# Kernel optimization log

Hardware: AMD Instinct MI355X
Metric: run time of the kernel (lower is better)

The kernel has to match this reference:

```python
import jax, jax.numpy as jnp
import numpy as np

DIM, H, DH, MLP, ADIM = 512, 8, 64, 2048, 256
B, T = 4, 2048
EPS = 1e-5


def setup_inputs() -> dict:
    key = jax.random.key(0)
    ks = jax.random.split(key, 10)
    s = 0.02
    inner = H * DH
    return {
        "x": jax.random.normal(ks[0], (B, T, DIM), jnp.float32),
        "action_emb": jax.random.normal(ks[1], (B, T, ADIM), jnp.float32),
        "causal_mask": jnp.tril(jnp.ones((T, T), dtype=bool)),
        "Wqkv": jax.random.normal(ks[2], (3 * inner, DIM), jnp.float32) * s,
        "Wout": jax.random.normal(ks[3], (DIM, inner), jnp.float32) * s,
        "bout": jnp.zeros((DIM,), jnp.float32),
        "W1": jax.random.normal(ks[4], (MLP, DIM), jnp.float32) * s,
        "b1": jnp.zeros((MLP,), jnp.float32),
        "W2": jax.random.normal(ks[5], (DIM, MLP), jnp.float32) * s,
        "b2": jnp.zeros((DIM,), jnp.float32),
        # adaLN is zero-init in the module; use small random so modulation is exercised
        "Wmod": jax.random.normal(ks[6], (6 * DIM, ADIM), jnp.float32) * s,
        "bmod": jnp.zeros((6 * DIM,), jnp.float32),
    }


def _layernorm(z):
    mu = jnp.mean(z, axis=-1, keepdims=True)
    var = jnp.var(z, axis=-1, keepdims=True)
    return (z - mu) * jax.lax.rsqrt(var + EPS)


def reference(x, action_emb, causal_mask, Wqkv, Wout, bout, W1, b1, W2, b2, Wmod, bmod):
    b, t, d = x.shape
    mod = jax.nn.silu(action_emb) @ Wmod.T + bmod            # (B,T,6*dim)
    shift1, scale1, gate1, shift2, scale2, gate2 = jnp.split(mod, 6, axis=-1)

    h = _layernorm(x) * (1.0 + scale1) + shift1
    qkv = (h @ Wqkv.T).reshape(b, t, 3, H, DH)
    q, k, v = qkv[:, :, 0], qkv[:, :, 1], qkv[:, :, 2]        # (B,T,H,DH)
    scores = jnp.einsum("bqhd,bkhd->bhqk", q, k) * (DH ** -0.5)
    scores = jnp.where(causal_mask, scores, -jnp.inf)
    attn = jax.nn.softmax(scores, axis=-1)                   # dropout=eval (identity)
    h = jnp.einsum("bhqk,bkhd->bqhd", attn, v).reshape(b, t, H * DH)
    h = h @ Wout.T + bout
    x = x + gate1 * h

    h = _layernorm(x) * (1.0 + scale2) + shift2
    h = jax.nn.gelu(h @ W1.T + b1, approximate=False) @ W2.T + b2
    return x + gate2 * h
```

## Files before the change

kernel.cpp:

```cpp
#include <hip/hip_runtime.h>
#include <math.h>
#include <stdint.h>

#define BB 4
#define TT 2048
#define NTOK 8192
#define DIMD 512
#define HH 8
#define DHH 64
#define MLPD 2048
#define ADIMD 256
#define MODD 3072
#define LNEPS 1e-5f
#define LOG2E_8 0.18033688011112042f

typedef short short8 __attribute__((ext_vector_type(8)));
typedef unsigned short ushort4v __attribute__((ext_vector_type(4)));
typedef __bf16 bf16x8 __attribute__((ext_vector_type(8)));
typedef float f32x4 __attribute__((ext_vector_type(4)));

static __device__ __forceinline__ unsigned short f2bf(float f) {
    union { float f; unsigned u; } v; v.f = f;
    unsigned r = v.u + 0x7fffu + ((v.u >> 16) & 1u);
    return (unsigned short)(r >> 16);
}
static __device__ __forceinline__ float bf2f(unsigned short u) {
    union { unsigned u; float f; } v; v.u = (unsigned)u << 16; return v.f;
}
static __device__ __forceinline__ unsigned pk2bf(float a, float b) {
    return (unsigned)f2bf(a) | ((unsigned)f2bf(b) << 16);
}

static __device__ __forceinline__ f32x4 mfma_bf16(short8 a, short8 b, f32x4 c) {
    return __builtin_amdgcn_mfma_f32_16x16x32_bf16(
        __builtin_bit_cast(bf16x8, a), __builtin_bit_cast(bf16x8, b), c, 0, 0, 0);
}

struct CvtArgs {
    const float* s[6];
    unsigned short* d[6];
    int cum[7];
};
__global__ __launch_bounds__(256) void cvt_all(CvtArgs a)
{
    const int i = blockIdx.x * 256 + threadIdx.x;
    if (i >= a.cum[6]) return;
    int seg = 0;
    #pragma unroll
    for (int k = 1; k < 6; k++) seg += (i >= a.cum[k]);
    const int off = i - a.cum[seg];
    float4 v = ((const float4*)a.s[seg])[off];
    if (seg == 5) {
        v.x = v.x / (1.f + __expf(-v.x));
        v.y = v.y / (1.f + __expf(-v.y));
        v.z = v.z / (1.f + __expf(-v.z));
        v.w = v.w / (1.f + __expf(-v.w));
    }
    uint2 o;
    o.x = pk2bf(v.x, v.y);
    o.y = pk2bf(v.z, v.w);
    ((uint2*)a.d[seg])[off] = o;
}

template<int EPI, int BN>
__global__ __launch_bounds__(256, (BN == 128 ? 3 : 4)) void gemm_bf16(
    const unsigned short* __restrict__ A, const unsigned short* __restrict__ Bw,
    const float* __restrict__ bias, const float* __restrict__ res,
    const unsigned short* __restrict__ mod,
    int M, int N, int K,
    void* __restrict__ Cv)
{
    constexpr int MT = (BN == 128) ? 4 : 2;
    constexpr int NPB = (BN == 128) ? 4 : 2;
    __shared__ unsigned short As[128 * 72];
    __shared__ unsigned short Bs[BN * 72];

    const int tid = threadIdx.x;
    const int w = tid >> 6, lane = tid & 63;
    const int quad = lane >> 4, l16 = lane & 15;
    const int wrow = (BN == 128) ? (w >> 1) * 64 : w * 32;
    const int wcol = (BN == 128) ? (w & 1) * 64 : 0;
    const int row0 = blockIdx.y * 128, col0 = blockIdx.x * BN;

    const int srow = tid >> 3;
    const int skc  = (tid & 7) * 8;

    f32x4 acc[MT][4];
    #pragma unroll
    for (int i = 0; i < MT; i++)
        #pragma unroll
        for (int j = 0; j < 4; j++) acc[i][j] = (f32x4){0.f, 0.f, 0.f, 0.f};

    short8 pA[4], pB[NPB];
    auto prefetch = [&](int k0) {
        #pragma unroll
        for (int p = 0; p < 4; p++)
            pA[p] = *(const short8*)&A[(size_t)(row0 + srow + p * 32) * K + k0 + skc];
        #pragma unroll
        for (int p = 0; p < NPB; p++)
            pB[p] = *(const short8*)&Bw[(size_t)(col0 + srow + p * 32) * K + k0 + skc];
    };
    auto stage = [&]() {
        #pragma unroll
        for (int p = 0; p < 4; p++)
            *(short8*)&As[(srow + p * 32) * 72 + skc] = pA[p];
        #pragma unroll
        for (int p = 0; p < NPB; p++)
            *(short8*)&Bs[(srow + p * 32) * 72 + skc] = pB[p];
    };

    prefetch(0);
    stage();
    __syncthreads();

    for (int k0 = 0; k0 < K; k0 += 64) {
        const bool more = (k0 + 64 < K);
        if (more) prefetch(k0 + 64);

        #pragma unroll
        for (int ks = 0; ks < 2; ks++) {
            short8 af[MT], bf[4];
            #pragma unroll
            for (int mt = 0; mt < MT; mt++)
                af[mt] = *(const short8*)&As[(wrow + mt * 16 + l16) * 72 + ks * 32 + quad * 8];
            #pragma unroll
            for (int nt = 0; nt < 4; nt++)
                bf[nt] = *(const short8*)&Bs[(wcol + nt * 16 + l16) * 72 + ks * 32 + quad * 8];
            #pragma unroll
            for (int nt = 0; nt < 4; nt++)
                #pragma unroll
                for (int mt = 0; mt < MT; mt++)
                    acc[mt][nt] = mfma_bf16(af[mt], bf[nt], acc[mt][nt]);
        }
        __syncthreads();
        if (more) stage();
        __syncthreads();
    }

    float* Cf = (float*)Cv;
    unsigned short* Cb = (unsigned short*)Cv;
    #pragma unroll
    for (int mt = 0; mt < MT; mt++) {
        #pragma unroll
        for (int r = 0; r < 4; r++) {
            const int row = row0 + wrow + mt * 16 + quad * 4 + r;
            #pragma unroll
            for (int nt = 0; nt < 4; nt++) {
                const int col = col0 + wcol + nt * 16 + l16;
                const size_t idx = (size_t)row * N + col;
                const float v = acc[mt][nt][r];
                if (EPI == 0) {
                    Cb[idx] = f2bf(v);
                } else if (EPI == 2) {
                    float t = v + bias[col];
                    Cb[idx] = f2bf(0.5f * t * (1.f + erff(t * 0.70710678118654752f)));
                } else if (EPI == 3) {
                    float t = v + bias[col];
                    Cf[idx] = res[idx] + bf2f(mod[(size_t)row * MODD + 1024 + col]) * t;
                } else if (EPI == 4) {
                    float t = v + bias[col];
                    Cf[idx] = Cf[idx] + bf2f(mod[(size_t)row * MODD + 2560 + col]) * t;
                } else if (EPI == 5) {
                    Cb[idx] = f2bf(v + bias[col]);
                }
            }
        }
    }
}

__global__ __launch_bounds__(256) void adaln_ln(
    const float* __restrict__ src, const unsigned short* __restrict__ mod,
    unsigned short* __restrict__ dst, int shift_off, int scale_off)
{
    const int n = blockIdx.x;
    const int tid = threadIdx.x;
    const float* xr = src + (size_t)n * DIMD;
    float v0 = xr[tid], v1 = xr[tid + 256];
    float s = v0 + v1;
    float q = v0 * v0 + v1 * v1;
    #pragma unroll
    for (int o = 32; o > 0; o >>= 1) {
        s += __shfl_down(s, o);
        q += __shfl_down(q, o);
    }
    __shared__ float sh[8];
    __shared__ float mu_sh, rs_sh;
    const int wid = tid >> 6, lane = tid & 63;
    if (lane == 0) { sh[wid] = s; sh[wid + 4] = q; }
    __syncthreads();
    if (tid == 0) {
        float S = sh[0] + sh[1] + sh[2] + sh[3];
        float Q = sh[4] + sh[5] + sh[6] + sh[7];
        float mu = S * (1.f / DIMD);
        float var = Q * (1.f / DIMD) - mu * mu;
        mu_sh = mu;
        rs_sh = rsqrtf(var + LNEPS);
    }
    __syncthreads();
    const float mu = mu_sh, rs = rs_sh;
    const unsigned short* mrow = mod + (size_t)n * MODD;
    const size_t o0 = (size_t)n * DIMD + tid;
    dst[o0]       = f2bf((v0 - mu) * rs * (1.f + bf2f(mrow[scale_off + tid]))       + bf2f(mrow[shift_off + tid]));
    dst[o0 + 256] = f2bf((v1 - mu) * rs * (1.f + bf2f(mrow[scale_off + tid + 256])) + bf2f(mrow[shift_off + tid + 256]));
}

__global__ __launch_bounds__(256, 4) void attn_mfma(
    const unsigned short* __restrict__ qkv, unsigned short* __restrict__ outb)
{
    __shared__ unsigned short Kt[64][72];
    __shared__ unsigned short Vt[64][72];
    __shared__ unsigned short Ps[4][16][72];

    const int qi = (TT / 64 - 1) - blockIdx.x;
    const int h = blockIdx.y, b = blockIdx.z;
    const int tid = threadIdx.x;
    const int w = tid >> 6;
    const int lane = tid & 63;
    const int quad = lane >> 4;
    const int l16 = lane & 15;

    const int qw = qi * 64 + w * 16;
    const size_t tokbase = (size_t)b * TT;

    short8 qf[2];
    {
        const unsigned short* qp = qkv + (tokbase + qw + l16) * 1536 + h * 64 + quad * 8;
        #pragma unroll
        for (int hd = 0; hd < 2; hd++) {
            short8 raw = *(const short8*)(qp + hd * 32);
            short8 f;
            #pragma unroll
            for (int j = 0; j < 8; j++)
                f[j] = (short)f2bf(bf2f((unsigned short)raw[j]) * LOG2E_8);
            qf[hd] = f;
        }
    }

    f32x4 Oa[4];
    float mrun = -INFINITY, lrun = 0.f;
    #pragma unroll
    for (int mt = 0; mt < 4; mt++) Oa[mt] = (f32x4){0.f, 0.f, 0.f, 0.f};

    const int nkt = qi + 1;
    const int vk0 = (tid & 31) * 2;
    const int vdb = (tid >> 5) * 8;

    short8 kpre[2], vpre[2];
    auto prefetchKV = [&](int kt) {
        const unsigned short* kb = qkv + (tokbase + (size_t)kt * 64) * 1536 + 512 + h * 64;
        #pragma unroll
        for (int it = 0; it < 2; it++) {
            const int i = tid + it * 256;
            kpre[it] = *(const short8*)(kb + (size_t)(i >> 3) * 1536 + (i & 7) * 8);
        }
        const unsigned short* vb = qkv + (tokbase + (size_t)kt * 64 + vk0) * 1536 + 1024 + h * 64 + vdb;
        vpre[0] = *(const short8*)vb;
        vpre[1] = *(const short8*)(vb + 1536);
    };
    auto storeKV = [&]() {
        #pragma unroll
        for (int it = 0; it < 2; it++) {
            const int i = tid + it * 256;
            *(short8*)&Kt[i >> 3][(i & 7) * 8] = kpre[it];
        }
        #pragma unroll
        for (int j = 0; j < 8; j++) {
            *(unsigned*)&Vt[vdb + j][vk0] =
                (unsigned)(unsigned short)vpre[0][j]
                | ((unsigned)(unsigned short)vpre[1][j] << 16);
        }
    };

    prefetchKV(0);
    storeKV();
    __syncthreads();

    for (int kt = 0; kt < nkt; kt++) {
        const bool haveNext = (kt + 1 < nkt);
        if (haveNext) prefetchKV(kt + 1);

        f32x4 st[4];
        #pragma unroll
        for (int mk = 0; mk < 4; mk++) {
            const short8 a0 = *(const short8*)&Kt[mk * 16 + l16][quad * 8];
            const short8 a1 = *(const short8*)&Kt[mk * 16 + l16][32 + quad * 8];
            st[mk] = (f32x4){0.f, 0.f, 0.f, 0.f};
            st[mk] = mfma_bf16(a0, qf[0], st[mk]);
            st[mk] = mfma_bf16(a1, qf[1], st[mk]);
        }
        if (kt == qi) {
            const int qpos = qw + l16;
            #pragma unroll
            for (int mk = 0; mk < 4; mk++)
                #pragma unroll
                for (int r = 0; r < 4; r++)
                    if (kt * 64 + mk * 16 + quad * 4 + r > qpos) st[mk][r] = -INFINITY;
        }
        float tm = -INFINITY;
        #pragma unroll
        for (int mk = 0; mk < 4; mk++)
            #pragma unroll
            for (int r = 0; r < 4; r++) tm = fmaxf(tm, st[mk][r]);
        tm = fmaxf(tm, __shfl_xor(tm, 16));
        tm = fmaxf(tm, __shfl_xor(tm, 32));
        const float mn = fmaxf(mrun, tm);
        const float alpha = __builtin_amdgcn_exp2f(mrun - mn);
        mrun = mn;
        float ts = 0.f;
        #pragma unroll
        for (int mk = 0; mk < 4; mk++) {
            const float p0 = __builtin_amdgcn_exp2f(st[mk][0] - mn);
            const float p1 = __builtin_amdgcn_exp2f(st[mk][1] - mn);
            const float p2 = __builtin_amdgcn_exp2f(st[mk][2] - mn);
            const float p3 = __builtin_amdgcn_exp2f(st[mk][3] - mn);
            ts += (p0 + p1) + (p2 + p3);
            const unsigned long long pk =
                (unsigned long long)pk2bf(p0, p1)
                | ((unsigned long long)pk2bf(p2, p3) << 32);
            *(unsigned long long*)&Ps[w][l16][mk * 16 + quad * 4] = pk;
        }
        ts += __shfl_xor(ts, 16);
        ts += __shfl_xor(ts, 32);
        lrun = lrun * alpha + ts;
        #pragma unroll
        for (int mt = 0; mt < 4; mt++) Oa[mt] *= alpha;
        __threadfence_block();

        short8 pf[2];
        #pragma unroll
        for (int kc = 0; kc < 2; kc++)
            pf[kc] = *(const short8*)&Ps[w][l16][kc * 32 + quad * 8];
        #pragma unroll
        for (int mt = 0; mt < 4; mt++)
            #pragma unroll
            for (int kc = 0; kc < 2; kc++) {
                const short8 vf = *(const short8*)&Vt[mt * 16 + l16][kc * 32 + quad * 8];
                Oa[mt] = mfma_bf16(vf, pf[kc], Oa[mt]);
            }

        __syncthreads();
        if (haveNext) storeKV();
        __syncthreads();
    }

    {
        const float inv = 1.f / lrun;
        const size_t tok = tokbase + qw + l16;
        #pragma unroll
        for (int mt = 0; mt < 4; mt++) {
            const unsigned long long pk =
                (unsigned long long)pk2bf(Oa[mt][0] * inv, Oa[mt][1] * inv)
                | ((unsigned long long)pk2bf(Oa[mt][2] * inv, Oa[mt][3] * inv) << 32);
            *(unsigned long long*)&outb[tok * DIMD + h * 64 + mt * 16 + quad * 4] = pk;
        }
    }
}

extern "C" void kernel_launch(void* const* d_in, const int* in_sizes, int n_in,
                              void* d_out, int out_size, void* d_ws, size_t ws_size,
                              hipStream_t stream)
{
    (void)in_sizes; (void)n_in; (void)out_size; (void)ws_size;

    const float* x    = (const float*)d_in[0];
    const float* aemb = (const float*)d_in[1];
    const float* Wqkv = (const float*)d_in[3];
    const float* Wout = (const float*)d_in[4];
    const float* bout = (const float*)d_in[5];
    const float* W1   = (const float*)d_in[6];
    const float* b1   = (const float*)d_in[7];
    const float* W2   = (const float*)d_in[8];
    const float* b2   = (const float*)d_in[9];
    const float* Wmod = (const float*)d_in[10];
    const float* bmod = (const float*)d_in[11];

    float* out = (float*)d_out;

    char* p = (char*)d_ws;
    unsigned short* modw = (unsigned short*)p; p += (size_t)NTOK * MODD * 2;
    unsigned short* h12  = (unsigned short*)p; p += (size_t)NTOK * DIMD * 2;
    unsigned short* qkvb = (unsigned short*)p; p += (size_t)NTOK * 1536 * 2;
    unsigned short* attw = (unsigned short*)p; p += (size_t)NTOK * DIMD * 2;
    unsigned short* hid  = qkvb;
    unsigned short* sact = (unsigned short*)p; p += (size_t)NTOK * ADIMD * 2;
    unsigned short* wq = (unsigned short*)p;   p += (size_t)1536 * 512 * 2;
    unsigned short* wo = (unsigned short*)p;   p += (size_t)512 * 512 * 2;
    unsigned short* w1 = (unsigned short*)p;   p += (size_t)2048 * 512 * 2;
    unsigned short* w2 = (unsigned short*)p;   p += (size_t)512 * 2048 * 2;
    unsigned short* wm = (unsigned short*)p;   p += (size_t)3072 * 256 * 2;

    CvtArgs ca;
    ca.s[0] = Wqkv; ca.d[0] = wq;
    ca.s[1] = Wout; ca.d[1] = wo;
    ca.s[2] = W1;   ca.d[2] = w1;
    ca.s[3] = W2;   ca.d[3] = w2;
    ca.s[4] = Wmod; ca.d[4] = wm;
    ca.s[5] = aemb; ca.d[5] = sact;
    const int n4s[6] = {1536 * 512 / 4, 512 * 512 / 4, 2048 * 512 / 4,
                        512 * 2048 / 4, 3072 * 256 / 4, NTOK * ADIMD / 4};
    ca.cum[0] = 0;
    for (int i = 0; i < 6; i++) ca.cum[i + 1] = ca.cum[i] + n4s[i];
    cvt_all<<<(ca.cum[6] + 255) / 256, 256, 0, stream>>>(ca);

    gemm_bf16<5, 128><<<dim3(MODD / 128, NTOK / 128), 256, 0, stream>>>(
        sact, wm, bmod, nullptr, nullptr, NTOK, MODD, ADIMD, modw);

    adaln_ln<<<NTOK, 256, 0, stream>>>(x, modw, h12, 0, 512);

    gemm_bf16<0, 128><<<dim3(1536 / 128, NTOK / 128), 256, 0, stream>>>(
        h12, wq, nullptr, nullptr, nullptr, NTOK, 1536, DIMD, qkvb);

    attn_mfma<<<dim3(TT / 64, HH, BB), 256, 0, stream>>>(qkvb, attw);

    gemm_bf16<3, 64><<<dim3(DIMD / 64, NTOK / 128), 256, 0, stream>>>(
        attw, wo, bout, x, modw, NTOK, DIMD, DIMD, out);

    adaln_ln<<<NTOK, 256, 0, stream>>>(out, modw, h12, 1536, 2048);

    gemm_bf16<2, 128><<<dim3(MLPD / 128, NTOK / 128), 256, 0, stream>>>(
        h12, w1, b1, nullptr, nullptr, NTOK, MLPD, DIMD, hid);

    gemm_bf16<4, 64><<<dim3(DIMD / 64, NTOK / 128), 256, 0, stream>>>(
        hid, w2, b2, nullptr, modw, NTOK, DIMD, MLPD, out);
}
```

Measured before the change: 330.7 us.

## Split causal attention KV range into chunks with a separate combine kernel

Each query tile's causal key range is split into chunks of up to 8 key tiles, giving 80 work items per (batch, head) instead of 32 tiles of very unequal length. Each chunk writes unnormalized fp32 partial outputs plus running max and sum to workspace, and a new combine kernel merges them with log-sum-exp rescaling into the bf16 attention output. The LDS row padding in the GEMM and attention kernels also changes from 72 to 76 to alter bank mapping. The split aims to cut the long tail from the longest causal rows, at the cost of extra fp32 partial traffic, an additional kernel launch, and possible misaligned 16-byte LDS accesses with the new stride.

```diff
diff --git a/kernel.cpp b/kernel.cpp
--- a/kernel.cpp
+++ b/kernel.cpp
@@ -13,6 +13,7 @@
 #define MODD 3072
 #define LNEPS 1e-5f
 #define LOG2E_8 0.18033688011112042f
+#define PBLK 4224
 
 typedef short short8 __attribute__((ext_vector_type(8)));
 typedef unsigned short ushort4v __attribute__((ext_vector_type(4)));
@@ -72,8 +73,8 @@
 {
     constexpr int MT = (BN == 128) ? 4 : 2;
     constexpr int NPB = (BN == 128) ? 4 : 2;
-    __shared__ unsigned short As[128 * 72];
-    __shared__ unsigned short Bs[BN * 72];
+    __shared__ unsigned short As[128 * 76];
+    __shared__ unsigned short Bs[BN * 76];
 
     const int tid = threadIdx.x;
     const int w = tid >> 6, lane = tid & 63;
@@ -103,10 +104,10 @@
     auto stage = [&]() {
         #pragma unroll
         for (int p = 0; p < 4; p++)
-            *(short8*)&As[(srow + p * 32) * 72 + skc] = pA[p];
+            *(short8*)&As[(srow + p * 32) * 76 + skc] = pA[p];
         #pragma unroll
         for (int p = 0; p < NPB; p++)
-            *(short8*)&Bs[(srow + p * 32) * 72 + skc] = pB[p];
+            *(short8*)&Bs[(srow + p * 32) * 76 + skc] = pB[p];
     };
 
     prefetch(0);
@@ -122,10 +123,10 @@
             short8 af[MT], bf[4];
             #pragma unroll
             for (int mt = 0; mt < MT; mt++)
-                af[mt] = *(const short8*)&As[(wrow + mt * 16 + l16) * 72 + ks * 32 + quad * 8];
+                af[mt] = *(const short8*)&As[(wrow + mt * 16 + l16) * 76 + ks * 32 + quad * 8];
             #pragma unroll
             for (int nt = 0; nt < 4; nt++)
-                bf[nt] = *(const short8*)&Bs[(wcol + nt * 16 + l16) * 72 + ks * 32 + quad * 8];
+                bf[nt] = *(const short8*)&Bs[(wcol + nt * 16 + l16) * 76 + ks * 32 + quad * 8];
             #pragma unroll
             for (int nt = 0; nt < 4; nt++)
                 #pragma unroll
@@ -205,13 +206,19 @@
 }
 
 __global__ __launch_bounds__(256, 4) void attn_mfma(
-    const unsigned short* __restrict__ qkv, unsigned short* __restrict__ outb)
-{
-    __shared__ unsigned short Kt[64][72];
-    __shared__ unsigned short Vt[64][72];
-    __shared__ unsigned short Ps[4][16][72];
-
-    const int qi = (TT / 64 - 1) - blockIdx.x;
+    const unsigned short* __restrict__ qkv, float* __restrict__ part)
+{
+    __shared__ unsigned short Kt[64][76];
+    __shared__ unsigned short Vt[64][76];
+    __shared__ unsigned short Ps[4][16][76];
+
+    const int f = 79 - (int)blockIdx.x;
+    int qi, ch;
+    if (f < 8)       { qi = f;               ch = 0; }
+    else if (f < 24) { const int g = f - 8;  qi = 8 + (g >> 1);  ch = g & 1; }
+    else if (f < 48) { const int g = f - 24; qi = 16 + g / 3;    ch = g % 3; }
+    else             { const int g = f - 48; qi = 24 + (g >> 2); ch = g & 3; }
+
     const int h = blockIdx.y, b = blockIdx.z;
     const int tid = threadIdx.x;
     const int w = tid >> 6;
@@ -228,11 +235,11 @@
         #pragma unroll
         for (int hd = 0; hd < 2; hd++) {
             short8 raw = *(const short8*)(qp + hd * 32);
-            short8 f;
+            short8 fr;
             #pragma unroll
             for (int j = 0; j < 8; j++)
-                f[j] = (short)f2bf(bf2f((unsigned short)raw[j]) * LOG2E_8);
-            qf[hd] = f;
+                fr[j] = (short)f2bf(bf2f((unsigned short)raw[j]) * LOG2E_8);
+            qf[hd] = fr;
         }
     }
 
@@ -241,7 +248,8 @@
     #pragma unroll
     for (int mt = 0; mt < 4; mt++) Oa[mt] = (f32x4){0.f, 0.f, 0.f, 0.f};
 
-    const int nkt = qi + 1;
+    const int k0t = ch * 8;
+    const int k1t = min(k0t + 8, qi + 1);
     const int vk0 = (tid & 31) * 2;
     const int vdb = (tid >> 5) * 8;
 
@@ -271,12 +279,12 @@
         }
     };
 
-    prefetchKV(0);
+    prefetchKV(k0t);
     storeKV();
     __syncthreads();
 
-    for (int kt = 0; kt < nkt; kt++) {
-        const bool haveNext = (kt + 1 < nkt);
+    for (int kt = k0t; kt < k1t; kt++) {
+        const bool haveNext = (kt + 1 < k1t);
         if (haveNext) prefetchKV(kt + 1);
 
         f32x4 st[4];
@@ -289,12 +297,12 @@
             st[mk] = mfma_bf16(a1, qf[1], st[mk]);
         }
         if (kt == qi) {
-            const int qpos = qw + l16;
+            const int qrel = w * 16 + l16;
             #pragma unroll
             for (int mk = 0; mk < 4; mk++)
                 #pragma unroll
                 for (int r = 0; r < 4; r++)
-                    if (kt * 64 + mk * 16 + quad * 4 + r > qpos) st[mk][r] = -INFINITY;
+                    if (mk * 16 + quad * 4 + r > qrel) st[mk][r] = -INFINITY;
         }
         float tm = -INFINITY;
         #pragma unroll
@@ -343,17 +351,52 @@
         __syncthreads();
     }
 
-    {
-        const float inv = 1.f / lrun;
-        const size_t tok = tokbase + qw + l16;
-        #pragma unroll
-        for (int mt = 0; mt < 4; mt++) {
-            const unsigned long long pk =
-                (unsigned long long)pk2bf(Oa[mt][0] * inv, Oa[mt][1] * inv)
-                | ((unsigned long long)pk2bf(Oa[mt][2] * inv, Oa[mt][3] * inv) << 32);
-            *(unsigned long long*)&outb[tok * DIMD + h * 64 + mt * 16 + quad * 4] = pk;
-        }
-    }
+    float* pO = part + ((size_t)((b * HH + h) * 80 + f)) * PBLK;
+    #pragma unroll
+    for (int mt = 0; mt < 4; mt++)
+        *(f32x4*)&pO[(w * 16 + l16) * 64 + mt * 16 + quad * 4] = Oa[mt];
+    if (quad == 0) {
+        pO[4096 + (w * 16 + l16) * 2]     = mrun;
+        pO[4096 + (w * 16 + l16) * 2 + 1] = lrun;
+    }
+}
+
+__global__ __launch_bounds__(256) void attn_combine(
+    const float* __restrict__ part, unsigned short* __restrict__ outb)
+{
+    const int idx = blockIdx.x * 256 + threadIdx.x;
+    const int d4 = idx & 15;
+    const int h = (idx >> 4) & 7;
+    const int tok = idx >> 7;
+    const int t = tok & (TT - 1);
+    const int b = tok >> 11;
+    const int qi = t >> 6;
+    const int nch = (qi >> 3) + 1;
+    int cum;
+    if (qi < 8)       cum = qi;
+    else if (qi < 16) cum = 8 + ((qi - 8) << 1);
+    else if (qi < 24) cum = 24 + (qi - 16) * 3;
+    else              cum = 48 + ((qi - 24) << 2);
+    const int qloc = t & 63;
+    const float* base = part + ((size_t)((b * HH + h) * 80 + cum)) * PBLK;
+
+    float M = -INFINITY;
+    for (int c = 0; c < nch; c++)
+        M = fmaxf(M, base[c * PBLK + 4096 + qloc * 2]);
+    float L = 0.f, a0 = 0.f, a1 = 0.f, a2 = 0.f, a3 = 0.f;
+    for (int c = 0; c < nch; c++) {
+        const float m = base[c * PBLK + 4096 + qloc * 2];
+        const float l = base[c * PBLK + 4097 + qloc * 2];
+        const float sc = __builtin_amdgcn_exp2f(m - M);
+        L += l * sc;
+        const float4 o = *(const float4*)&base[c * PBLK + qloc * 64 + d4 * 4];
+        a0 += sc * o.x; a1 += sc * o.y; a2 += sc * o.z; a3 += sc * o.w;
+    }
+    const float inv = 1.f / L;
+    const unsigned long long pk =
+        (unsigned long long)pk2bf(a0 * inv, a1 * inv)
+        | ((unsigned long long)pk2bf(a2 * inv, a3 * inv) << 32);
+    *(unsigned long long*)&outb[(size_t)tok * DIMD + h * 64 + d4 * 4] = pk;
 }
 
 extern "C" void kernel_launch(void* const* d_in, const int* in_sizes, int n_in,
@@ -388,6 +431,8 @@
     unsigned short* w1 = (unsigned short*)p;   p += (size_t)2048 * 512 * 2;
     unsigned short* w2 = (unsigned short*)p;   p += (size_t)512 * 2048 * 2;
     unsigned short* wm = (unsigned short*)p;   p += (size_t)3072 * 256 * 2;
+    p = (char*)(((uintptr_t)p + 255) & ~(uintptr_t)255);
+    float* part = (float*)p;
 
     CvtArgs ca;
     ca.s[0] = Wqkv; ca.d[0] = wq;
@@ -410,7 +455,8 @@
     gemm_bf16<0, 128><<<dim3(1536 / 128, NTOK / 128), 256, 0, stream>>>(
         h12, wq, nullptr, nullptr, nullptr, NTOK, 1536, DIMD, qkvb);
 
-    attn_mfma<<<dim3(TT / 64, HH, BB), 256, 0, stream>>>(qkvb, attw);
+    attn_mfma<<<dim3(80, HH, BB), 256, 0, stream>>>(qkvb, part);
+    attn_combine<<<NTOK * HH * 16 / 256, 256, 0, stream>>>(part, attw);
 
     gemm_bf16<3, 64><<<dim3(DIMD / 64, NTOK / 128), 256, 0, stream>>>(
         attw, wo, bout, x, modw, NTOK, DIMD, DIMD, out);
```

Result: faster. 320.9 us (-3.0%).
